# Optimization experiments

Hardware: AMD Instinct MI355X
Metric: run time of the kernel (lower is better)

The kernel has to match this reference:

```python
import jax, jax.numpy as jnp
import numpy as np

N = 50000          # num nodes
E = 800000         # num edges (avg degree 16)
D_IN = 128         # input_size
H = 128            # hidden_size
BN_EPS = 1e-5


def setup_inputs() -> dict:
    key = jax.random.key(0)
    ks = jax.random.split(key, 16)
    std = 1.0 / np.sqrt(H)
    u = lambda k, shape: jax.random.uniform(k, shape, jnp.float32, -std, std)
    return {
        "x": jax.random.normal(ks[0], (N, D_IN), jnp.float32),
        "hx": jax.random.normal(ks[1], (N, H), jnp.float32),
        "cx": jax.random.normal(ks[2], (N, H), jnp.float32),
        "edge_src": jax.random.randint(ks[3], (E,), 0, N, jnp.int32),
        "edge_dst": jax.random.randint(ks[4], (E,), 0, N, jnp.int32),
        "edge_weight": jax.random.uniform(ks[5], (E,), jnp.float32) / 16.0,  # ~normalized adj values
        "gcn_weight": u(ks[6], (D_IN, H)),
        "bias": u(ks[7], (H,)),
        "x2h_w": u(ks[8], (4 * H, H)),
        "x2h_b": u(ks[9], (4 * H,)),
        "h2h_w": u(ks[10], (4 * H, H)),
        "h2h_b": u(ks[11], (4 * H,)),
        "bn_gamma": u(ks[12], (H,)),
        "bn_beta": u(ks[13], (H,)),
        "bn_mean": jnp.zeros((H,), jnp.float32),
        "bn_var": jnp.ones((H,), jnp.float32),
    }


def reference(x, hx, cx, edge_src, edge_dst, edge_weight, gcn_weight, bias,
              x2h_w, x2h_b, h2h_w, h2h_b, bn_gamma, bn_beta, bn_mean, bn_var):
    # GCN: support = x @ W, then sparse adj @ support via gather/segment-sum
    support = x @ gcn_weight                                   # (N, H)
    msgs = edge_weight[:, None] * support[edge_src]            # (E, H)
    agg = jax.ops.segment_sum(msgs, edge_dst, num_segments=N)  # (N, H) = spmm(adj, support)
    h = jax.nn.relu(agg)
    # dropout: eval mode -> identity
    h = h + bias
    # BatchNorm1d (eval mode, running stats)
    h = (h - bn_mean) * jax.lax.rsqrt(bn_var + BN_EPS) * bn_gamma + bn_beta
    # fused LSTM gates: x2h(h) + h2h(hx)
    gates = h @ x2h_w.T + x2h_b + hx @ h2h_w.T + h2h_b         # (N, 4H)
    i_g, f_g, g_g, o_g = jnp.split(gates, 4, axis=1)
    cy = cx * jax.nn.sigmoid(f_g) + jax.nn.sigmoid(i_g) * jnp.tanh(g_g)
    hy = jax.nn.sigmoid(o_g) * jnp.tanh(cy)
    return hy, cy
```

## Files before the change

kernel.cpp:

```cpp
#include <hip/hip_runtime.h>

#define NN 50000
#define NE 800000
#define HH 128
#define BN_EPS 1e-5f
#define SCAN_NB ((NN + 255) / 256)
#define PREP_NB 512
#define EPB 2048
#define HIST_NB ((NE + EPB - 1) / EPB)
#define SCAT_NB ((NE + EPB - 1) / EPB)
#define SUPP_NB ((NN + 63) / 64)

typedef unsigned short u16;
typedef unsigned int u32;
typedef short bf16x8 __attribute__((ext_vector_type(8)));
typedef float f32x4 __attribute__((ext_vector_type(4)));

static __device__ __forceinline__ float bf2f(u16 u){
  union { u32 i; float f; } v; v.i = ((u32)u) << 16; return v.f;
}
static __device__ __forceinline__ u16 f2bf(float f){
  union { float f; u32 i; } v; v.f = f;
  u32 x = v.i;
  return (u16)((x + 0x7fffu + ((x >> 16) & 1u)) >> 16);
}
static __device__ __forceinline__ float sigm(float x){
  return 1.f / (1.f + __expf(-x));
}
static __device__ __forceinline__ float tanh_fast(float x){
  return 1.f - 2.f / (1.f + __expf(2.f * x));
}

__global__ __launch_bounds__(256) void fused_prep_hist(
    const float* __restrict__ x2hw, const float* __restrict__ h2hw,
    const float* __restrict__ x2hb, const float* __restrict__ h2hb,
    const float* __restrict__ gcnw,
    u16* __restrict__ wcat, u16* __restrict__ wgcn, float* __restrict__ bsum,
    const int* __restrict__ edst, int* __restrict__ counts){
  int bid = blockIdx.x;
  if (bid < PREP_NB){
    int i = bid * 256 + threadIdx.x;
    int n = i >> 8, k = i & 255;
    float v = (k < 128) ? x2hw[n * 128 + k] : h2hw[n * 128 + (k - 128)];
    int nt = n >> 4, lc = n & 15;
    int kk = k >> 5, lq = (k >> 3) & 3, e = k & 7;
    wcat[(((nt * 8 + kk) * 64) + lq * 16 + lc) * 8 + e] = f2bf(v);
    if (i < 16384){
      int nn = i >> 7, kx = i & 127;
      wgcn[i] = f2bf(gcnw[kx * 128 + nn]);
    }
    if (i < 512) bsum[i] = x2hb[i] + h2hb[i];
  } else {
    int base = (bid - PREP_NB) * EPB + threadIdx.x * 8;
    if (base + 8 <= NE){
      int4 d0 = *(const int4*)(edst + base);
      int4 d1 = *(const int4*)(edst + base + 4);
      atomicAdd(&counts[d0.x], 1); atomicAdd(&counts[d0.y], 1);
      atomicAdd(&counts[d0.z], 1); atomicAdd(&counts[d0.w], 1);
      atomicAdd(&counts[d1.x], 1); atomicAdd(&counts[d1.y], 1);
      atomicAdd(&counts[d1.z], 1); atomicAdd(&counts[d1.w], 1);
    } else {
      for (int e = base; e < NE; e++) atomicAdd(&counts[edst[e]], 1);
    }
  }
}


__global__ __launch_bounds__(256) void scan_bsum(
    const int* __restrict__ counts, int* __restrict__ bsums, int n){
  int i = blockIdx.x * 256 + threadIdx.x;
  int v = (i < n) ? counts[i] : 0;
#pragma unroll
  for (int off = 1; off < 64; off <<= 1) v += __shfl_xor(v, off);
  __shared__ int ws[4];
  if ((threadIdx.x & 63) == 0) ws[threadIdx.x >> 6] = v;
  __syncthreads();
  if (threadIdx.x == 0) bsums[blockIdx.x] = ws[0] + ws[1] + ws[2] + ws[3];
}

__global__ __launch_bounds__(256) void scan_final2(
    const int* __restrict__ counts, const int* __restrict__ bsums,
    int* __restrict__ offs, int* __restrict__ cursor, int n, int nb){
  __shared__ int sh[256], bs[256];
  int t = threadIdx.x;
  int bv = (t < nb) ? bsums[t] : 0;
  bs[t] = bv;
  __syncthreads();
  for (int off = 1; off < 256; off <<= 1){
    int u = (t >= off) ? bs[t - off] : 0;
    __syncthreads();
    bs[t] += u;
    __syncthreads();
  }
  int bexcl = (blockIdx.x > 0) ? bs[blockIdx.x - 1] : 0;
  int i = blockIdx.x * 256 + t;
  int v = (i < n) ? counts[i] : 0;
  sh[t] = v;
  __syncthreads();
  for (int off = 1; off < 256; off <<= 1){
    int u = (t >= off) ? sh[t - off] : 0;
    __syncthreads();
    sh[t] += u;
    __syncthreads();
  }
  int excl = sh[t] - v + bexcl;
  if (i < n){ offs[i] = excl; cursor[i] = excl; }
}

__global__ __launch_bounds__(256) void fused_support_scatter(
    const float* __restrict__ x, const u16* __restrict__ wgcn,
    u16* __restrict__ support,
    const int* __restrict__ src, const int* __restrict__ dst,
    const float* __restrict__ w, int* __restrict__ cursor, int2* __restrict__ esw,
    int N){
  int bid = blockIdx.x;
  if (bid >= SUPP_NB){
    int base = (bid - SUPP_NB) * EPB + threadIdx.x * 8;
    if (base + 8 <= NE){
      int4 d0 = *(const int4*)(dst + base);
      int4 d1 = *(const int4*)(dst + base + 4);
      int4 s0 = *(const int4*)(src + base);
      int4 s1 = *(const int4*)(src + base + 4);
      float4 w0 = *(const float4*)(w + base);
      float4 w1 = *(const float4*)(w + base + 4);
      int   d[8] = {d0.x, d0.y, d0.z, d0.w, d1.x, d1.y, d1.z, d1.w};
      int   s[8] = {s0.x, s0.y, s0.z, s0.w, s1.x, s1.y, s1.z, s1.w};
      float g[8] = {w0.x, w0.y, w0.z, w0.w, w1.x, w1.y, w1.z, w1.w};
      int pos[8];
#pragma unroll
      for (int k = 0; k < 8; k++) pos[k] = atomicAdd(&cursor[d[k]], 1);
#pragma unroll
      for (int k = 0; k < 8; k++) esw[pos[k]] = make_int2(s[k], __float_as_int(g[k]));
    } else {
      for (int e = base; e < NE; e++){
        int pos = atomicAdd(&cursor[dst[e]], 1);
        esw[pos] = make_int2(src[e], __float_as_int(w[e]));
      }
    }
    return;
  }
  int tid = threadIdx.x;
  int wave = tid >> 6, lane = tid & 63;
  int c = lane & 15, q = lane >> 4;
  int row0 = bid * 64 + wave * 16;
  int arow = row0 + c; if (arow > N - 1) arow = N - 1;
  f32x4 acc[8];
#pragma unroll
  for (int t = 0; t < 8; t++) acc[t] = (f32x4){0.f, 0.f, 0.f, 0.f};

  const u16* wp = wgcn + (size_t)c * 128 + q * 8;
#pragma unroll
  for (int k0 = 0; k0 < 128; k0 += 32){
    const float* ap = x + (size_t)arow * 128 + k0 + q * 8;
    float4 f0 = *(const float4*)ap;
    float4 f1 = *(const float4*)(ap + 4);
    u16 tmp[8] = {f2bf(f0.x), f2bf(f0.y), f2bf(f0.z), f2bf(f0.w),
                  f2bf(f1.x), f2bf(f1.y), f2bf(f1.z), f2bf(f1.w)};
    bf16x8 afrag = *(bf16x8*)tmp;
#pragma unroll
    for (int t = 0; t < 8; t++){
      bf16x8 bfrag = *(const bf16x8*)(wp + (size_t)t * 16 * 128 + k0);
      acc[t] = __builtin_amdgcn_mfma_f32_16x16x32_bf16(afrag, bfrag, acc[t], 0, 0, 0);
    }
  }
#pragma unroll
  for (int t = 0; t < 8; t++){
#pragma unroll
    for (int j = 0; j < 4; j++){
      int r = row0 + q * 4 + j;
      if (r < N) support[(size_t)r * 128 + t * 16 + c] = f2bf(acc[t][j]);
    }
  }
}

__global__ __launch_bounds__(256) void agg_bn3(
    const u16* __restrict__ support, const int2* __restrict__ esw,
    const int* __restrict__ offs, const int* __restrict__ counts,
    const float* __restrict__ bias, const float* __restrict__ gamma,
    const float* __restrict__ beta, const float* __restrict__ mean,
    const float* __restrict__ var, const float* __restrict__ hx,
    u16* __restrict__ hbn, u16* __restrict__ hxb, int N){
  int wid = blockIdx.x * 4 + (threadIdx.x >> 6);
  int lane = threadIdx.x & 63;
  if (wid >= N) return;
  int c = lane * 2;
  float2 hv = *(const float2*)(hx + (size_t)wid * HH + c);
  int start = offs[wid];
  int deg   = counts[wid];
  float a0 = 0.f, a1 = 0.f;
  int e = 0;
  for (; e + 8 <= deg; e += 8){
    int2 ev[8]; u32 u[8];
#pragma unroll
    for (int k = 0; k < 8; k++) ev[k] = esw[start + e + k];
#pragma unroll
    for (int k = 0; k < 8; k++)
      u[k] = *(const u32*)(support + (size_t)ev[k].x * HH + c);
#pragma unroll
    for (int k = 0; k < 8; k++){
      float g = __int_as_float(ev[k].y);
      a0 = fmaf(g, bf2f((u16)(u[k] & 0xffffu)), a0);
      a1 = fmaf(g, bf2f((u16)(u[k] >> 16)), a1);
    }
  }
  for (; e + 4 <= deg; e += 4){
    int2 ev[4]; u32 u[4];
#pragma unroll
    for (int k = 0; k < 4; k++) ev[k] = esw[start + e + k];
#pragma unroll
    for (int k = 0; k < 4; k++)
      u[k] = *(const u32*)(support + (size_t)ev[k].x * HH + c);
#pragma unroll
    for (int k = 0; k < 4; k++){
      float g = __int_as_float(ev[k].y);
      a0 = fmaf(g, bf2f((u16)(u[k] & 0xffffu)), a0);
      a1 = fmaf(g, bf2f((u16)(u[k] >> 16)), a1);
    }
  }
  for (; e < deg; e++){
    int2 ev = esw[start + e];
    float g = __int_as_float(ev.y);
    u32 ui = *(const u32*)(support + (size_t)ev.x * HH + c);
    a0 = fmaf(g, bf2f((u16)(ui & 0xffffu)), a0);
    a1 = fmaf(g, bf2f((u16)(ui >> 16)), a1);
  }
  float h0 = fmaxf(a0, 0.f) + bias[c];
  float h1 = fmaxf(a1, 0.f) + bias[c + 1];
  float s0 = gamma[c]     * rsqrtf(var[c]     + BN_EPS);
  float s1 = gamma[c + 1] * rsqrtf(var[c + 1] + BN_EPS);
  float r0 = (h0 - mean[c])     * s0 + beta[c];
  float r1 = (h1 - mean[c + 1]) * s1 + beta[c + 1];
  u32 pack = (u32)f2bf(r0) | ((u32)f2bf(r1) << 16);
  *(u32*)(hbn + (size_t)wid * HH + c) = pack;
  u32 hp = (u32)f2bf(hv.x) | ((u32)f2bf(hv.y) << 16);
  *(u32*)(hxb + (size_t)wid * HH + c) = hp;
}

__global__ __launch_bounds__(512, 4) void gates_mfma7(
    const u16* __restrict__ hbn, const u16* __restrict__ hxb,
    const u16* __restrict__ wcat, const float* __restrict__ bsum,
    const float* __restrict__ cx, float* __restrict__ out, int N){
  __shared__ float lbuf[2][4][16][64];
  int tid = threadIdx.x;
  int wave = tid >> 6, lane = tid & 63;
  int c = lane & 15, q = lane >> 4;
  int cw = wave & 3, kh = wave >> 2;
  int hh = blockIdx.y;
  int hloc = hh * 64 + cw * 16 + c;

  const bf16x8* wsrc = (const bf16x8*)wcat;
  bf16x8 btile[4][4];
#pragma unroll
  for (int g = 0; g < 4; g++)
#pragma unroll
    for (int kk = 0; kk < 4; kk++)
      btile[g][kk] = wsrc[((size_t)((g * 8 + hh * 4 + cw) * 8) + kh * 4 + kk) * 64 + lane];

  float bi = 0.f, bf_ = 0.f, bg = 0.f, bo = 0.f;
  if (kh == 0){
    bi  = bsum[hloc];
    bf_ = bsum[128 + hloc];
    bg  = bsum[256 + hloc];
    bo  = bsum[384 + hloc];
  }
  const u16* abuf = kh ? hxb : hbn;
  const size_t NH = (size_t)N * HH;
  const int nchunk = N >> 4;
  int p = 0;
  int chunk = blockIdx.x;

  bf16x8 a_cur[4];
  if (chunk < nchunk){
    const u16* ap = abuf + (size_t)((chunk << 4) + c) * 128 + q * 8;
#pragma unroll
    for (int kk = 0; kk < 4; kk++) a_cur[kk] = *(const bf16x8*)(ap + kk * 32);
  }

  for (; chunk < nchunk; chunk += gridDim.x){
    int row0 = chunk << 4;
    int nxt = chunk + gridDim.x;
    int prow = (nxt < nchunk) ? (nxt << 4) : 0;
    const u16* pnp = abuf + (size_t)(prow + c) * 128 + q * 8;
    bf16x8 a_nxt[4];
#pragma unroll
    for (int kk = 0; kk < 4; kk++) a_nxt[kk] = *(const bf16x8*)(pnp + kk * 32);
    float cxv[4];
    if (kh == 0){
#pragma unroll
      for (int j = 0; j < 4; j++)
        cxv[j] = cx[(size_t)(row0 + q * 4 + j) * HH + hloc];
    }

    f32x4 acc[4];
#pragma unroll
    for (int g = 0; g < 4; g++) acc[g] = (f32x4){0.f, 0.f, 0.f, 0.f};
#pragma unroll
    for (int kk = 0; kk < 4; kk++){
#pragma unroll
      for (int g = 0; g < 4; g++)
        acc[g] = __builtin_amdgcn_mfma_f32_16x16x32_bf16(a_cur[kk], btile[g][kk], acc[g], 0, 0, 0);
    }
    if (kh == 1){
#pragma unroll
      for (int g = 0; g < 4; g++)
#pragma unroll
        for (int j = 0; j < 4; j++)
          lbuf[p][cw][g * 4 + j][lane] = acc[g][j];
    }
    __syncthreads();
    if (kh == 0){
#pragma unroll
      for (int j = 0; j < 4; j++){
        int r = row0 + q * 4 + j;
        float gi = acc[0][j] + lbuf[p][cw][0 + j][lane]  + bi;
        float gf = acc[1][j] + lbuf[p][cw][4 + j][lane]  + bf_;
        float gg = acc[2][j] + lbuf[p][cw][8 + j][lane]  + bg;
        float go = acc[3][j] + lbuf[p][cw][12 + j][lane] + bo;
        float is = sigm(gi), fs = sigm(gf), gt = tanh_fast(gg), os = sigm(go);
        float cyv = cxv[j] * fs + is * gt;
        out[(size_t)r * HH + hloc]      = os * tanh_fast(cyv);
        out[NH + (size_t)r * HH + hloc] = cyv;
      }
    }
#pragma unroll
    for (int kk = 0; kk < 4; kk++) a_cur[kk] = a_nxt[kk];
    p ^= 1;
  }
}


extern "C" void kernel_launch(void* const* d_in, const int* in_sizes, int n_in,
                              void* d_out, int out_size, void* d_ws, size_t ws_size,
                              hipStream_t stream){
  const float* x     = (const float*)d_in[0];
  const float* hx    = (const float*)d_in[1];
  const float* cx    = (const float*)d_in[2];
  const int*   esrc  = (const int*)d_in[3];
  const int*   edst  = (const int*)d_in[4];
  const float* ew    = (const float*)d_in[5];
  const float* gcn_w = (const float*)d_in[6];
  const float* bias  = (const float*)d_in[7];
  const float* x2hw  = (const float*)d_in[8];
  const float* x2hb  = (const float*)d_in[9];
  const float* h2hw  = (const float*)d_in[10];
  const float* h2hb  = (const float*)d_in[11];
  const float* bn_g  = (const float*)d_in[12];
  const float* bn_b  = (const float*)d_in[13];
  const float* bn_m  = (const float*)d_in[14];
  const float* bn_v  = (const float*)d_in[15];
  float* out = (float*)d_out;

  char* w = (char*)d_ws;
  u16* support = (u16*)w; w += (((size_t)NN * HH * 2) + 255) & ~(size_t)255;
  u16* hbn     = (u16*)w; w += (((size_t)NN * HH * 2) + 255) & ~(size_t)255;
  u16* hxb     = (u16*)w; w += (((size_t)NN * HH * 2) + 255) & ~(size_t)255;
  int* counts  = (int*)w; w += (((size_t)NN * 4) + 255) & ~(size_t)255;
  int* offs    = (int*)w; w += (((size_t)NN * 4) + 255) & ~(size_t)255;
  int* cursor  = (int*)w; w += (((size_t)NN * 4) + 255) & ~(size_t)255;
  int* bsums   = (int*)w; w += (((size_t)SCAN_NB * 4) + 255) & ~(size_t)255;
  int2* esw    = (int2*)w; w += (((size_t)NE * 8) + 255) & ~(size_t)255;
  u16* wcat    = (u16*)w; w += (((size_t)512 * 256 * 2) + 255) & ~(size_t)255;
  u16* wgcn    = (u16*)w; w += (((size_t)128 * 128 * 2) + 255) & ~(size_t)255;
  float* bsum  = (float*)w; w += (((size_t)512 * 4) + 255) & ~(size_t)255;

  hipMemsetAsync(counts, 0, (size_t)NN * 4, stream);
  fused_prep_hist<<<PREP_NB + HIST_NB, 256, 0, stream>>>(
      x2hw, h2hw, x2hb, h2hb, gcn_w, wcat, wgcn, bsum, edst, counts);
  scan_bsum<<<SCAN_NB, 256, 0, stream>>>(counts, bsums, NN);
  scan_final2<<<SCAN_NB, 256, 0, stream>>>(counts, bsums, offs, cursor, NN, SCAN_NB);
  fused_support_scatter<<<SUPP_NB + SCAT_NB, 256, 0, stream>>>(
      x, wgcn, support, esrc, edst, ew, cursor, esw, NN);
  agg_bn3<<<(NN + 3) / 4, 256, 0, stream>>>(support, esw, offs, counts,
                                            bias, bn_g, bn_b, bn_m, bn_v, hx, hbn, hxb, NN);
  gates_mfma7<<<dim3(256, 2), 512, 0, stream>>>(hbn, hxb, wcat, bsum, cx, out, NN);
}
```

Before: 337.5 us.

## Drop split-K LDS reduction in gates kernel; each wave handles full K

Each wave in the gates kernel now covers the full 256-wide K dimension (both the h and hx halves), with doubled B tiles held in registers. This removes the shared-memory partial-sum exchange and the per-chunk __syncthreads between the two K-halves. Blocks shrink to 256 threads and the grid doubles in x. The cost is higher register pressure (32 B tiles plus 8 A fragments per lane) and possibly lower occupancy.

```diff
diff --git a/kernel.cpp b/kernel.cpp
--- a/kernel.cpp
+++ b/kernel.cpp
@@ -236,95 +236,84 @@
   *(u32*)(hxb + (size_t)wid * HH + c) = hp;
 }
 
-__global__ __launch_bounds__(512, 4) void gates_mfma7(
+__global__ __launch_bounds__(256, 2) void gates_mfma8(
     const u16* __restrict__ hbn, const u16* __restrict__ hxb,
     const u16* __restrict__ wcat, const float* __restrict__ bsum,
     const float* __restrict__ cx, float* __restrict__ out, int N){
-  __shared__ float lbuf[2][4][16][64];
   int tid = threadIdx.x;
   int wave = tid >> 6, lane = tid & 63;
   int c = lane & 15, q = lane >> 4;
-  int cw = wave & 3, kh = wave >> 2;
   int hh = blockIdx.y;
-  int hloc = hh * 64 + cw * 16 + c;
+  int ct = hh * 4 + wave;
+  int hloc = ct * 16 + c;
 
   const bf16x8* wsrc = (const bf16x8*)wcat;
-  bf16x8 btile[4][4];
+  bf16x8 btile[4][8];
 #pragma unroll
   for (int g = 0; g < 4; g++)
 #pragma unroll
-    for (int kk = 0; kk < 4; kk++)
-      btile[g][kk] = wsrc[((size_t)((g * 8 + hh * 4 + cw) * 8) + kh * 4 + kk) * 64 + lane];
-
-  float bi = 0.f, bf_ = 0.f, bg = 0.f, bo = 0.f;
-  if (kh == 0){
-    bi  = bsum[hloc];
-    bf_ = bsum[128 + hloc];
-    bg  = bsum[256 + hloc];
-    bo  = bsum[384 + hloc];
-  }
-  const u16* abuf = kh ? hxb : hbn;
+    for (int kk = 0; kk < 8; kk++)
+      btile[g][kk] = wsrc[((size_t)((g * 8 + ct) * 8) + kk) * 64 + lane];
+
+  float bi  = bsum[hloc];
+  float bf_ = bsum[128 + hloc];
+  float bg  = bsum[256 + hloc];
+  float bo  = bsum[384 + hloc];
   const size_t NH = (size_t)N * HH;
   const int nchunk = N >> 4;
-  int p = 0;
   int chunk = blockIdx.x;
 
-  bf16x8 a_cur[4];
-  if (chunk < nchunk){
-    const u16* ap = abuf + (size_t)((chunk << 4) + c) * 128 + q * 8;
-#pragma unroll
-    for (int kk = 0; kk < 4; kk++) a_cur[kk] = *(const bf16x8*)(ap + kk * 32);
+  bf16x8 a_cur[8];
+  {
+    const u16* ap0 = hbn + (size_t)((chunk << 4) + c) * 128 + q * 8;
+    const u16* ap1 = hxb + (size_t)((chunk << 4) + c) * 128 + q * 8;
+#pragma unroll
+    for (int kk = 0; kk < 4; kk++){
+      a_cur[kk]     = *(const bf16x8*)(ap0 + kk * 32);
+      a_cur[4 + kk] = *(const bf16x8*)(ap1 + kk * 32);
+    }
   }
 
   for (; chunk < nchunk; chunk += gridDim.x){
     int row0 = chunk << 4;
     int nxt = chunk + gridDim.x;
     int prow = (nxt < nchunk) ? (nxt << 4) : 0;
-    const u16* pnp = abuf + (size_t)(prow + c) * 128 + q * 8;
-    bf16x8 a_nxt[4];
-#pragma unroll
-    for (int kk = 0; kk < 4; kk++) a_nxt[kk] = *(const bf16x8*)(pnp + kk * 32);
+    const u16* pn0 = hbn + (size_t)(prow + c) * 128 + q * 8;
+    const u16* pn1 = hxb + (size_t)(prow + c) * 128 + q * 8;
+    bf16x8 a_nxt[8];
+#pragma unroll
+    for (int kk = 0; kk < 4; kk++){
+      a_nxt[kk]     = *(const bf16x8*)(pn0 + kk * 32);
+      a_nxt[4 + kk] = *(const bf16x8*)(pn1 + kk * 32);
+    }
     float cxv[4];
-    if (kh == 0){
-#pragma unroll
-      for (int j = 0; j < 4; j++)
-        cxv[j] = cx[(size_t)(row0 + q * 4 + j) * HH + hloc];
-    }
+#pragma unroll
+    for (int j = 0; j < 4; j++)
+      cxv[j] = cx[(size_t)(row0 + q * 4 + j) * HH + hloc];
 
     f32x4 acc[4];
 #pragma unroll
     for (int g = 0; g < 4; g++) acc[g] = (f32x4){0.f, 0.f, 0.f, 0.f};
 #pragma unroll
-    for (int kk = 0; kk < 4; kk++){
+    for (int kk = 0; kk < 8; kk++){
 #pragma unroll
       for (int g = 0; g < 4; g++)
         acc[g] = __builtin_amdgcn_mfma_f32_16x16x32_bf16(a_cur[kk], btile[g][kk], acc[g], 0, 0, 0);
     }
-    if (kh == 1){
-#pragma unroll
-      for (int g = 0; g < 4; g++)
-#pragma unroll
-        for (int j = 0; j < 4; j++)
-          lbuf[p][cw][g * 4 + j][lane] = acc[g][j];
-    }
-    __syncthreads();
-    if (kh == 0){
-#pragma unroll
-      for (int j = 0; j < 4; j++){
-        int r = row0 + q * 4 + j;
-        float gi = acc[0][j] + lbuf[p][cw][0 + j][lane]  + bi;
-        float gf = acc[1][j] + lbuf[p][cw][4 + j][lane]  + bf_;
-        float gg = acc[2][j] + lbuf[p][cw][8 + j][lane]  + bg;
-        float go = acc[3][j] + lbuf[p][cw][12 + j][lane] + bo;
-        float is = sigm(gi), fs = sigm(gf), gt = tanh_fast(gg), os = sigm(go);
-        float cyv = cxv[j] * fs + is * gt;
-        out[(size_t)r * HH + hloc]      = os * tanh_fast(cyv);
-        out[NH + (size_t)r * HH + hloc] = cyv;
-      }
-    }
-#pragma unroll
-    for (int kk = 0; kk < 4; kk++) a_cur[kk] = a_nxt[kk];
-    p ^= 1;
+#pragma unroll
+    for (int j = 0; j < 4; j++){
+      int r = row0 + q * 4 + j;
+      float gi = acc[0][j] + bi;
+      float gf = acc[1][j] + bf_;
+      float gg = acc[2][j] + bg;
+      float go = acc[3][j] + bo;
+      float is = sigm(gi), fs = sigm(gf), gt = tanh_fast(gg), os = sigm(go);
+      float cyv = cxv[j] * fs + is * gt;
+      out[(size_t)r * HH + hloc]      = os * tanh_fast(cyv);
+      out[NH + (size_t)r * HH + hloc] = cyv;
+    }
+#pragma unroll
+    for (int kk = 0; kk < 8; kk++) a_cur[kk] = a_nxt[kk];
   }
 }
 
@@ -372,5 +361,5 @@
       x, wgcn, support, esrc, edst, ew, cursor, esw, NN);
   agg_bn3<<<(NN + 3) / 4, 256, 0, stream>>>(support, esw, offs, counts,
                                             bias, bn_g, bn_b, bn_m, bn_v, hx, hbn, hxb, NN);
-  gates_mfma7<<<dim3(256, 2), 512, 0, stream>>>(hbn, hxb, wcat, bsum, cx, out, NN);
-}
+  gates_mfma8<<<dim3(512, 2), 256, 0, stream>>>(hbn, hxb, wcat, bsum, cx, out, NN);
+}
```

Result: no change. 331.2 us (-1.9%).
